# Performance work log

Measured on AMD Instinct MI355X. Metric: run time of the kernel, lower is better.

The kernel has to match this reference:

```python
import jax, jax.numpy as jnp
import numpy as np

K = 4  # neighbors per node (loop=False, PyG knn_graph default)

def _leaky(x):
    return jax.nn.leaky_relu(x, negative_slope=0.01)

def _knn(pos):
    # pos: [B, N, 3]. k nearest neighbors per node within its own graph, no self-loops.
    d = jnp.sum((pos[:, :, None, :] - pos[:, None, :, :]) ** 2, axis=-1)  # [B, N, N]
    n = pos.shape[1]
    d = jnp.where(jnp.eye(n, dtype=bool), jnp.inf, d)
    _, idx = jax.lax.top_k(-d, K)
    return idx  # [B, N, K] neighbor (source) indices per center node

def _edge_conv(x, idx, w1, b1, w2, b2):
    # PyG EdgeConv, aggr='add': out_i = sum_j MLP(concat[x_i, x_j - x_i])
    xj = jax.vmap(lambda xb, ib: xb[ib])(x, idx)  # gather neighbors -> [B, N, K, F]
    xi = x[:, :, None, :]
    e = jnp.concatenate([jnp.broadcast_to(xi, xj.shape), xj - xi], axis=-1)  # [B,N,K,2F]
    h = _leaky(_leaky(e @ w1 + b1) @ w2 + b2)
    return h.sum(axis=2)  # scatter-add over the K neighbors -> [B, N, F_out]

# l1=4, l2=96, l3=192, l4=252, l5=192, l6=96, l7=1  (input_size=4, c=3, output_size=1)
PARAM_SHAPES = [
    ("c1w1", (8, 96)), ("c1b1", (96,)), ("c1w2", (96, 192)), ("c1b2", (192,)),
    ("c2w1", (384, 252)), ("c2b1", (252,)), ("c2w2", (252, 192)), ("c2b2", (192,)),
    ("c3w1", (384, 252)), ("c3b1", (252,)), ("c3w2", (252, 192)), ("c3b2", (192,)),
    ("c4w1", (384, 252)), ("c4b1", (252,)), ("c4w2", (252, 192)), ("c4b2", (192,)),
    ("nn1w", (772, 252)), ("nn1b", (252,)),
    ("nn2w", (252, 192)), ("nn2b", (192,)),
    ("nn3w", (768, 96)), ("nn3b", (96,)),
    ("nn4w", (96, 1)), ("nn4b", (1,)),
]

def setup_inputs():
    key = jax.random.key(0)
    B, N, F = 256, 256, 4  # 256 graphs x 256 nodes, 4 node features
    inp = {"x": jax.random.normal(key, (B, N, F), jnp.float32)}
    for i, (name, shp) in enumerate(PARAM_SHAPES):
        k = jax.random.fold_in(key, i + 1)
        scale = 1.0 / np.sqrt(shp[0]) if len(shp) == 2 else 0.01
        inp[name] = jax.random.normal(k, shp, jnp.float32) * scale
    return inp

def reference(x, c1w1, c1b1, c1w2, c1b2, c2w1, c2b1, c2w2, c2b2,
              c3w1, c3b1, c3w2, c3b2, c4w1, c4b1, c4w2, c4b2,
              nn1w, nn1b, nn2w, nn2b, nn3w, nn3b, nn4w, nn4b):
    # 4 rounds of (dynamic kNN on first 3 feature cols) + EdgeConv(add)
    a = _edge_conv(x, _knn(x[..., :3]), c1w1, c1b1, c1w2, c1b2)
    b = _edge_conv(a, _knn(a[..., :3]), c2w1, c2b1, c2w2, c2b2)
    c = _edge_conv(b, _knn(b[..., :3]), c3w1, c3b1, c3w2, c3b2)
    d = _edge_conv(c, _knn(c[..., :3]), c4w1, c4b1, c4w2, c4b2)
    h = jnp.concatenate([x, a, b, c, d], axis=-1)  # [B, N, 4 + 4*192 = 772]
    h = _leaky(h @ nn1w + nn1b)
    h = h @ nn2w + nn2b  # [B, N, 192]
    # four-way global pooling per graph: max / min / sum / mean
    pooled = jnp.concatenate(
        [h.max(axis=1), h.min(axis=1), h.sum(axis=1), h.mean(axis=1)], axis=-1)  # [B, 768]
    out = _leaky(pooled)
    out = _leaky(out @ nn3w + nn3b)
    return out @ nn4w + nn4b  # [B, 1] (mode='custom': no tanh)
```

## Files before the change

### kernel.cpp

```cpp
#include <hip/hip_runtime.h>
#include <cstdint>
#include <cstddef>

#define LK(x) ((x) > 0.f ? (x) : 0.01f * (x))

typedef _Float16 f16x8 __attribute__((ext_vector_type(8)));
typedef _Float16 f16x4 __attribute__((ext_vector_type(4)));
typedef float f32x4 __attribute__((ext_vector_type(4)));

constexpr int B_ = 256;
constexpr int N_ = 256;
constexpr int BN = B_ * N_;
constexpr int CHUNK_B = 64;
constexpr int CHUNK_ROWS = CHUNK_B * N_;

__device__ inline void dec2(float v, _Float16& h, _Float16& l) {
  _Float16 hh = (_Float16)v;
  h = hh;
  l = (_Float16)(v - (float)hh);
}

__global__ void knn_kernel(const float* __restrict__ feat, int F, int* __restrict__ idxout) {
  __shared__ float px[N_], py[N_], pz[N_];
  int b = blockIdx.x, t = threadIdx.x;
  const float* row = feat + ((size_t)b * N_ + t) * F;
  px[t] = row[0]; py[t] = row[1]; pz[t] = row[2];
  __syncthreads();
  float x = px[t], y = py[t], z = pz[t];
  float bd0 = INFINITY, bd1 = INFINITY, bd2 = INFINITY, bd3 = INFINITY;
  int bi0 = 0, bi1 = 0, bi2 = 0, bi3 = 0;
  for (int j = 0; j < N_; ++j) {
    #pragma clang fp contract(off)
    float dx = x - px[j], dy = y - py[j], dz = z - pz[j];
    float d = (dx * dx + dy * dy) + dz * dz;
    if (j == t) continue;
    if (d < bd3) {
      if (d < bd2) {
        bd3 = bd2; bi3 = bi2;
        if (d < bd1) {
          bd2 = bd1; bi2 = bi1;
          if (d < bd0) { bd1 = bd0; bi1 = bi0; bd0 = d; bi0 = j; }
          else         { bd1 = d; bi1 = j; }
        } else         { bd2 = d; bi2 = j; }
      } else           { bd3 = d; bi3 = j; }
    }
  }
  int* o = idxout + ((size_t)b * N_ + t) * 4;
  o[0] = bi0; o[1] = bi1; o[2] = bi2; o[3] = bi3;
}


__global__ void prep_uvw(const float* __restrict__ w1, const float* __restrict__ b1,
                         int F, int H1, float* __restrict__ wcat, float* __restrict__ bcat) {
  int t = blockIdx.x * 256 + threadIdx.x;
  int FH = F * H1;
  if (t < FH) {
    int k = t / H1, c = t - k * H1;
    float top = w1[(size_t)k * H1 + c];
    float bot = w1[(size_t)(F + k) * H1 + c];
    wcat[(size_t)k * 2 * H1 + c]      = top - bot;
    wcat[(size_t)k * 2 * H1 + H1 + c] = bot;
  }
  if (t < H1) { bcat[t] = b1[t]; bcat[H1 + t] = 0.f; }
}

template<bool ACT_A, bool ACCUM, bool HAS_BIAS>
__global__ __launch_bounds__(256) void gemm_f32(
    const float* __restrict__ A, const float* __restrict__ W,
    const float* __restrict__ bias, float* __restrict__ C,
    int M, int N, int K) {
  __shared__ float sA[16][132];
  __shared__ float sW[16][68];
  int tid = threadIdx.x;
  int m0 = blockIdx.y * 128;
  int n0 = blockIdx.x * 64;
  int kkA = tid & 15, mA = tid >> 4;
  int nW = tid & 63, kW = tid >> 6;
  int ty = tid >> 4, tx = tid & 15;
  float acc[8][4] = {};
  for (int k0 = 0; k0 < K; k0 += 16) {
    int kg = k0 + kkA;
    #pragma unroll
    for (int i = 0; i < 8; ++i) {
      int m = mA + i * 16;
      float v = 0.f;
      if (kg < K) {
        v = A[(size_t)(m0 + m) * K + kg];
        if (ACT_A) v = LK(v);
      }
      sA[kkA][m] = v;
    }
    #pragma unroll
    for (int q = 0; q < 4; ++q) {
      int kk = kW + q * 4;
      int kgw = k0 + kk, n = n0 + nW;
      float v = 0.f;
      if (kgw < K && n < N) v = W[(size_t)kgw * N + n];
      sW[kk][nW] = v;
    }
    __syncthreads();
    #pragma unroll
    for (int kk = 0; kk < 16; ++kk) {
      float4 a0 = *(const float4*)&sA[kk][ty * 8];
      float4 a1 = *(const float4*)&sA[kk][ty * 8 + 4];
      float4 w  = *(const float4*)&sW[kk][tx * 4];
      float av[8] = {a0.x, a0.y, a0.z, a0.w, a1.x, a1.y, a1.z, a1.w};
      float wv[4] = {w.x, w.y, w.z, w.w};
      #pragma unroll
      for (int i = 0; i < 8; ++i)
        #pragma unroll
        for (int j = 0; j < 4; ++j)
          acc[i][j] += av[i] * wv[j];
    }
    __syncthreads();
  }
  int n = n0 + tx * 4;
  float bv[4] = {0.f, 0.f, 0.f, 0.f};
  if (HAS_BIAS) {
    #pragma unroll
    for (int j = 0; j < 4; ++j) if (n + j < N) bv[j] = bias[n + j];
  }
  #pragma unroll
  for (int i = 0; i < 8; ++i) {
    size_t m = (size_t)(m0 + ty * 8 + i);
    if (n + 3 < N) {
      float4 o;
      o.x = acc[i][0] + bv[0]; o.y = acc[i][1] + bv[1];
      o.z = acc[i][2] + bv[2]; o.w = acc[i][3] + bv[3];
      float4* cp = (float4*)(C + m * N + n);
      if (ACCUM) { float4 c = *cp; o.x += c.x; o.y += c.y; o.z += c.z; o.w += c.w; }
      *cp = o;
    } else {
      #pragma unroll
      for (int j = 0; j < 4; ++j) {
        if (n + j < N) {
          float v = acc[i][j] + bv[j];
          size_t off = m * N + n + j;
          if (ACCUM) v += C[off];
          C[off] = v;
        }
      }
    }
  }
}

__global__ __launch_bounds__(256) void edge_stage2(
    const float* __restrict__ UV, const int* __restrict__ idx,
    const float* __restrict__ w2, const float* __restrict__ b2,
    float* __restrict__ out, int H1) {
  __shared__ float sH[16][68];
  __shared__ float sW[16][196];
  __shared__ int sJ[64];
  int tid = threadIdx.x;
  int g0 = blockIdx.x * 16;
  int bbase = (g0 >> 8) << 8;
  if (tid < 64) sJ[tid] = bbase + idx[(size_t)g0 * 4 + tid];
  int W2 = H1 * 2;
  int r = tid >> 2, seg = tid & 3;
  int gp_r = g0 + (r >> 2);
  int ty = tid >> 4, tx = tid & 15;
  int gp = g0 + ty;
  float acc[4][12] = {};
  int nKt = (H1 + 15) >> 4;
  for (int kt = 0; kt < nKt; ++kt) {
    int k0 = kt << 4;
    __syncthreads();
    {
      int c = k0 + (seg << 2);
      const float* up = UV + (size_t)gp_r * W2 + c;
      const float* vp = UV + (size_t)sJ[r] * W2 + H1 + c;
      float u[4], v[4];
      if (c + 3 < H1) {
        float4 uu = *(const float4*)up; float4 vv = *(const float4*)vp;
        u[0] = uu.x; u[1] = uu.y; u[2] = uu.z; u[3] = uu.w;
        v[0] = vv.x; v[1] = vv.y; v[2] = vv.z; v[3] = vv.w;
      } else {
        #pragma unroll
        for (int j = 0; j < 4; ++j) {
          u[j] = (c + j < H1) ? up[j] : 0.f;
          v[j] = (c + j < H1) ? vp[j] : 0.f;
        }
      }
      #pragma unroll
      for (int j = 0; j < 4; ++j) {
        float t = u[j] + v[j];
        sH[(seg << 2) + j][r] = (c + j < H1) ? LK(t) : 0.f;
      }
    }
    #pragma unroll
    for (int p = 0; p < 3; ++p) {
      int q = tid + (p << 8);
      int kk = q / 48;
      int c4 = q - kk * 48;
      int k = k0 + kk;
      float4 wv = {0.f, 0.f, 0.f, 0.f};
      if (k < H1) wv = *(const float4*)(w2 + (size_t)k * 192 + (c4 << 2));
      *(float4*)&sW[kk][c4 << 2] = wv;
    }
    __syncthreads();
    #pragma unroll
    for (int kk = 0; kk < 16; ++kk) {
      float4 a = *(const float4*)&sH[kk][ty << 2];
      float av[4] = {a.x, a.y, a.z, a.w};
      #pragma unroll
      for (int ct = 0; ct < 3; ++ct) {
        float4 w = *(const float4*)&sW[kk][ct * 64 + (tx << 2)];
        float wv[4] = {w.x, w.y, w.z, w.w};
        #pragma unroll
        for (int i = 0; i < 4; ++i)
          #pragma unroll
          for (int j = 0; j < 4; ++j)
            acc[i][ct * 4 + j] += av[i] * wv[j];
      }
    }
  }
  #pragma unroll
  for (int ct = 0; ct < 3; ++ct) {
    float o[4];
    #pragma unroll
    for (int j = 0; j < 4; ++j) {
      int col = ct * 64 + (tx << 2) + j;
      float bvv = b2[col];
      float s = 0.f;
      #pragma unroll
      for (int i = 0; i < 4; ++i) {
        float t = acc[i][ct * 4 + j] + bvv;
        s += LK(t);
      }
      o[j] = s;
    }
    float4 ov = {o[0], o[1], o[2], o[3]};
    *(float4*)(out + (size_t)gp * 192 + ct * 64 + (tx << 2)) = ov;
  }
}


__global__ void prep_wcatT(const float* __restrict__ w1, const float* __restrict__ b1,
                           int F, int H1, int Fpad, _Float16* __restrict__ Wp,
                           float* __restrict__ bcat) {
  int t = blockIdx.x * 256 + threadIdx.x;
  int NN = 2 * H1;
  if (t < NN * Fpad) {
    int n = t / Fpad, k = t - n * Fpad;
    float v = 0.f;
    if (k < F) {
      if (n < H1) v = w1[(size_t)k * H1 + n] - w1[(size_t)(F + k) * H1 + n];
      else        v = w1[(size_t)(F + k) * H1 + (n - H1)];
    }
    _Float16 h, l; dec2(v, h, l);
    size_t base = (size_t)n * 2 * Fpad + (size_t)(k >> 3) * 16 + (k & 7);
    Wp[base] = h; Wp[base + 8] = l;
  }
  if (t < NN) bcat[t] = (t < H1) ? b1[t] : 0.f;
}

__global__ void prep_wT(const float* __restrict__ W, int K, int N, int Kpad,
                        _Float16* __restrict__ Wp) {
  int t = blockIdx.x * 256 + threadIdx.x;
  if (t >= N * Kpad) return;
  int n = t / Kpad, k = t - n * Kpad;
  float v = (k < K) ? W[(size_t)k * N + n] : 0.f;
  _Float16 h, l; dec2(v, h, l);
  size_t base = (size_t)n * 2 * Kpad + (size_t)(k >> 3) * 16 + (k & 7);
  Wp[base] = h; Wp[base + 8] = l;
}

template<bool ACT_A, bool ACCUM, bool HAS_BIAS>
__global__ __launch_bounds__(256) void gemm3h(
    const float* __restrict__ A0, const float* __restrict__ A1, int w0,
    const _Float16* __restrict__ Wp, const float* __restrict__ bias,
    float* __restrict__ C, int M, int N, int K, int Kpad) {
  __shared__ _Float16 sA[128 * 72];
  __shared__ _Float16 sB[128 * 72];
  int tid = threadIdx.x;
  int m0 = blockIdx.y * 128, n0 = blockIdx.x * 128;
  int lane = tid & 63, wid = tid >> 6;
  int wy = wid >> 1, wx = wid & 1;
  int lm = lane & 15, lq = lane >> 4;
  int rA = tid >> 1, qA = (tid & 1) * 4;
  f32x4 acc[4][4];
  #pragma unroll
  for (int i = 0; i < 4; ++i)
    #pragma unroll
    for (int j = 0; j < 4; ++j) acc[i][j] = 0.f;

  for (int k0 = 0; k0 < Kpad; k0 += 32) {
    __syncthreads();
    {
      const float* Ap; int kb, wA;
      if (k0 < w0) { Ap = A0; kb = k0;      wA = w0; }
      else         { Ap = A1; kb = k0 - w0; wA = K - w0; }
      const float* arow = Ap + (size_t)(m0 + rA) * wA;
      #pragma unroll
      for (int qi = 0; qi < 4; ++qi) {
        int q = qA + qi;
        int kl = kb + q * 4;
        float4 v = {0.f, 0.f, 0.f, 0.f};
        if (kl + 3 < wA) v = *(const float4*)(arow + kl);
        else {
          if (kl + 0 < wA) v.x = arow[kl + 0];
          if (kl + 1 < wA) v.y = arow[kl + 1];
          if (kl + 2 < wA) v.z = arow[kl + 2];
        }
        if (ACT_A) { v.x = LK(v.x); v.y = LK(v.y); v.z = LK(v.z); v.w = LK(v.w); }
        _Float16 h0,h1,h2,h3,l0,l1,l2,l3;
        dec2(v.x,h0,l0); dec2(v.y,h1,l1); dec2(v.z,h2,l2); dec2(v.w,h3,l3);
        int off = rA * 72 + (q >> 1) * 16 + (q & 1) * 4;
        f16x4 th; th[0]=h0; th[1]=h1; th[2]=h2; th[3]=h3;
        f16x4 tl; tl[0]=l0; tl[1]=l1; tl[2]=l2; tl[3]=l3;
        *(f16x4*)&sA[off]     = th;
        *(f16x4*)&sA[off + 8] = tl;
      }
    }
    {
      int n = n0 + rA;
      const _Float16* src = Wp + (size_t)n * 2 * Kpad + (size_t)k0 * 2;
      #pragma unroll
      for (int ui = 0; ui < 4; ++ui) {
        int u = (tid & 1) * 4 + ui;
        float4 v = {0.f, 0.f, 0.f, 0.f};
        if (n < N) v = *(const float4*)(src + u * 8);
        *(float4*)&sB[rA * 72 + u * 8] = v;
      }
    }
    __syncthreads();
    f16x8 af[4][2], bf[4][2];
    #pragma unroll
    for (int mt = 0; mt < 4; ++mt) {
      int row = wy * 64 + mt * 16 + lm;
      af[mt][0] = *(const f16x8*)&sA[row * 72 + lq * 16];
      af[mt][1] = *(const f16x8*)&sA[row * 72 + lq * 16 + 8];
    }
    #pragma unroll
    for (int nt = 0; nt < 4; ++nt) {
      int row = wx * 64 + nt * 16 + lm;
      bf[nt][0] = *(const f16x8*)&sB[row * 72 + lq * 16];
      bf[nt][1] = *(const f16x8*)&sB[row * 72 + lq * 16 + 8];
    }
    #pragma unroll
    for (int mt = 0; mt < 4; ++mt)
      #pragma unroll
      for (int nt = 0; nt < 4; ++nt) {
        acc[mt][nt] = __builtin_amdgcn_mfma_f32_16x16x32_f16(af[mt][0], bf[nt][0], acc[mt][nt], 0, 0, 0);
        acc[mt][nt] = __builtin_amdgcn_mfma_f32_16x16x32_f16(af[mt][0], bf[nt][1], acc[mt][nt], 0, 0, 0);
        acc[mt][nt] = __builtin_amdgcn_mfma_f32_16x16x32_f16(af[mt][1], bf[nt][0], acc[mt][nt], 0, 0, 0);
      }
  }
  #pragma unroll
  for (int mt = 0; mt < 4; ++mt) {
    #pragma unroll
    for (int nt = 0; nt < 4; ++nt) {
      int n = n0 + wx * 64 + nt * 16 + lm;
      if (n >= N) continue;
      float bv = HAS_BIAS ? bias[n] : 0.f;
      #pragma unroll
      for (int r = 0; r < 4; ++r) {
        size_t m = (size_t)m0 + wy * 64 + mt * 16 + lq * 4 + r;
        float v = acc[mt][nt][r] + bv;
        size_t off = m * N + n;
        if (ACCUM) v += C[off];
        C[off] = v;
      }
    }
  }
}

__global__ __launch_bounds__(256) void edge_stage2_m(
    const float* __restrict__ UV, const int* __restrict__ idx,
    const _Float16* __restrict__ Wp, const float* __restrict__ b2,
    float* __restrict__ out, int H1, int Kpad) {
  __shared__ _Float16 sH[64 * 72];
  __shared__ _Float16 sW[192 * 72];
  __shared__ int sJ[64];
  int tid = threadIdx.x;
  int g0 = blockIdx.x * 16;
  int bbase = (g0 >> 8) << 8;
  if (tid < 64) sJ[tid] = bbase + idx[(size_t)g0 * 4 + tid];
  int W2 = 2 * H1;
  int lane = tid & 63, w = tid >> 6;
  int lm = lane & 15, lq = lane >> 4;
  int rS = tid >> 2, qS = tid & 3;
  f32x4 acc[4][3];
  #pragma unroll
  for (int i = 0; i < 4; ++i)
    #pragma unroll
    for (int j = 0; j < 3; ++j) acc[i][j] = 0.f;

  for (int k0 = 0; k0 < Kpad; k0 += 32) {
    __syncthreads();
    {
      int gp_r = g0 + (rS >> 2);
      int jr = sJ[rS];
      const float* up = UV + (size_t)gp_r * W2;
      const float* vp = UV + (size_t)jr * W2 + H1;
      #pragma unroll
      for (int hf = 0; hf < 2; ++hf) {
        int k = k0 + qS * 8 + hf * 4;
        float4 u = {0.f,0.f,0.f,0.f}, v = {0.f,0.f,0.f,0.f};
        if (k + 3 < H1) { u = *(const float4*)(up + k); v = *(const float4*)(vp + k); }
        else {
          if (k + 0 < H1) { u.x = up[k+0]; v.x = vp[k+0]; }
          if (k + 1 < H1) { u.y = up[k+1]; v.y = vp[k+1]; }
          if (k + 2 < H1) { u.z = up[k+2]; v.z = vp[k+2]; }
        }
        float e0 = LK(u.x + v.x), e1 = LK(u.y + v.y), e2 = LK(u.z + v.z), e3 = LK(u.w + v.w);
        _Float16 h0,h1,h2,h3,l0,l1,l2,l3;
        dec2(e0,h0,l0); dec2(e1,h1,l1); dec2(e2,h2,l2); dec2(e3,h3,l3);
        int off = rS * 72 + qS * 16 + hf * 4;
        f16x4 th; th[0]=h0; th[1]=h1; th[2]=h2; th[3]=h3;
        f16x4 tl; tl[0]=l0; tl[1]=l1; tl[2]=l2; tl[3]=l3;
        *(f16x4*)&sH[off]     = th;
        *(f16x4*)&sH[off + 8] = tl;
      }
    }
    {
      const _Float16* src = Wp + (size_t)k0 * 2;
      #pragma unroll
      for (int p = 0; p < 6; ++p) {
        int e = tid + p * 256;
        int n = e >> 3, u = e & 7;
        *(float4*)&sW[n * 72 + u * 8] =
            *(const float4*)(src + (size_t)n * 2 * Kpad + u * 8);
      }
    }
    __syncthreads();
    f16x8 af[4][2], bf[3][2];
    #pragma unroll
    for (int mt = 0; mt < 4; ++mt) {
      int row = mt * 16 + lm;
      af[mt][0] = *(const f16x8*)&sH[row * 72 + lq * 16];
      af[mt][1] = *(const f16x8*)&sH[row * 72 + lq * 16 + 8];
    }
    #pragma unroll
    for (int t3 = 0; t3 < 3; ++t3) {
      int row = (w * 3 + t3) * 16 + lm;
      bf[t3][0] = *(const f16x8*)&sW[row * 72 + lq * 16];
      bf[t3][1] = *(const f16x8*)&sW[row * 72 + lq * 16 + 8];
    }
    #pragma unroll
    for (int mt = 0; mt < 4; ++mt)
      #pragma unroll
      for (int t3 = 0; t3 < 3; ++t3) {
        acc[mt][t3] = __builtin_amdgcn_mfma_f32_16x16x32_f16(af[mt][0], bf[t3][0], acc[mt][t3], 0, 0, 0);
        acc[mt][t3] = __builtin_amdgcn_mfma_f32_16x16x32_f16(af[mt][0], bf[t3][1], acc[mt][t3], 0, 0, 0);
        acc[mt][t3] = __builtin_amdgcn_mfma_f32_16x16x32_f16(af[mt][1], bf[t3][0], acc[mt][t3], 0, 0, 0);
      }
  }
  #pragma unroll
  for (int mt = 0; mt < 4; ++mt) {
    int gp = g0 + mt * 4 + lq;
    #pragma unroll
    for (int t3 = 0; t3 < 3; ++t3) {
      int col = (w * 3 + t3) * 16 + lm;
      float bv = b2[col];
      float s = 0.f;
      #pragma unroll
      for (int r = 0; r < 4; ++r) s += LK(acc[mt][t3][r] + bv);
      out[(size_t)gp * 192 + col] = s;
    }
  }
}

__global__ __launch_bounds__(256) void nn1_init(const float* __restrict__ x,
                                                const float* __restrict__ Wx,
                                                const float* __restrict__ b,
                                                float* __restrict__ h1) {
  __shared__ float sX[64][4];
  __shared__ float sW[4][256];
  int tid = threadIdx.x;
  int r0 = blockIdx.x * 64;
  if (tid < 64) *(float4*)sX[tid] = *(const float4*)(x + (size_t)(r0 + tid) * 4);
  for (int e = tid; e < 1024; e += 256) {
    int k = e >> 8, n = e & 255;
    sW[k][n] = (n < 252) ? Wx[(size_t)k * 252 + n] : 0.f;
  }
  __syncthreads();
  int cg = tid & 63, rr = tid >> 6;
  if (cg < 63) {
    #pragma unroll 4
    for (int i = 0; i < 16; ++i) {
      int rl = rr + i * 4;
      float x0 = sX[rl][0], x1 = sX[rl][1], x2 = sX[rl][2], x3 = sX[rl][3];
      float4 o;
      int c = cg * 4;
      o.x = b[c+0] + x0*sW[0][c+0] + x1*sW[1][c+0] + x2*sW[2][c+0] + x3*sW[3][c+0];
      o.y = b[c+1] + x0*sW[0][c+1] + x1*sW[1][c+1] + x2*sW[2][c+1] + x3*sW[3][c+1];
      o.z = b[c+2] + x0*sW[0][c+2] + x1*sW[1][c+2] + x2*sW[2][c+2] + x3*sW[3][c+2];
      o.w = b[c+3] + x0*sW[0][c+3] + x1*sW[1][c+3] + x2*sW[2][c+3] + x3*sW[3][c+3];
      *(float4*)(h1 + (size_t)(r0 + rl) * 252 + c) = o;
    }
  }
}

__global__ void pool_kernel(const float* __restrict__ h, float* __restrict__ pooled) {
  int b = blockIdx.x, ch = threadIdx.x;
  const float* p = h + (size_t)b * N_ * 192 + ch;
  float mx = -INFINITY, mn = INFINITY, sm = 0.f;
  for (int n = 0; n < N_; ++n) {
    float v = p[(size_t)n * 192];
    mx = fmaxf(mx, v); mn = fminf(mn, v); sm += v;
  }
  float* o = pooled + (size_t)b * 768;
  o[ch]       = LK(mx);
  o[192 + ch] = LK(mn);
  o[384 + ch] = LK(sm);
  o[576 + ch] = LK(sm * (1.f / 256.f));
}

__global__ void head_kernel(const float* __restrict__ pooled,
                            const float* __restrict__ w3, const float* __restrict__ b3,
                            const float* __restrict__ w4, const float* __restrict__ b4,
                            float* __restrict__ out) {
  __shared__ float sp[768];
  __shared__ float st[96];
  int b = blockIdx.x, t = threadIdx.x;
  for (int c = t; c < 768; c += 128) sp[c] = pooled[(size_t)b * 768 + c];
  __syncthreads();
  if (t < 96) {
    float s = b3[t];
    for (int r = 0; r < 768; ++r) s += sp[r] * w3[(size_t)r * 96 + t];
    s = LK(s);
    st[t] = s * w4[t];
  }
  __syncthreads();
  if (t == 0) {
    float s = b4[0];
    for (int i = 0; i < 96; ++i) s += st[i];
    out[b] = s;
  }
}

extern "C" void kernel_launch(void* const* d_in, const int* in_sizes, int n_in,
                              void* d_out, int out_size, void* d_ws, size_t ws_size,
                              hipStream_t stream) {
  (void)in_sizes; (void)n_in; (void)out_size; (void)ws_size;
  const float* x = (const float*)d_in[0];
  const float* P[25];
  for (int i = 0; i < 25; ++i) P[i] = (const float*)d_in[i];

  char* ws = (char*)d_ws;
  int*       idx    = (int*)      (ws + 0);
  float*     A      = (float*)    (ws + 1048576);
  float*     Bb     = (float*)    (ws + 51380224);
  float*     h1     = (float*)    (ws + 101711872);
  float*     UV     = (float*)    (ws + 167772160);
  float*     pooled = (float*)    (ws + 200802304);
  char*      WSH1   =             (ws + 201588736);
  _Float16*  WB2    = (_Float16*) (ws + 202113024);
  float*     bcat   = (float*)    (ws + 202637312);

  float*    wcat = (float*)   WSH1;
  _Float16* WB1  = (_Float16*)WSH1;

  auto edge_layer_f32 = [&](const float* src, int F, int H1,
                            const float* w1, const float* b1,
                            const float* w2, const float* b2, float* dst) {
    knn_kernel<<<B_, N_, 0, stream>>>(src, F, idx);
    prep_uvw<<<(F * H1 + 255) / 256, 256, 0, stream>>>(w1, b1, F, H1, wcat, bcat);
    int W2 = 2 * H1;
    dim3 gUV((W2 + 63) / 64, CHUNK_ROWS / 128);
    for (int cb = 0; cb < B_; cb += CHUNK_B) {
      size_t base = (size_t)cb * N_;
      gemm_f32<false, false, true><<<gUV, 256, 0, stream>>>(src + base * F, wcat, bcat, UV, CHUNK_ROWS, W2, F);
      edge_stage2<<<CHUNK_ROWS / 16, 256, 0, stream>>>(UV, idx + base * 4, w2, b2, dst + base * 192, H1);
    }
  };

  auto edge_layer_f16 = [&](const float* src, int F, int H1,
                            const float* w1, const float* b1,
                            const float* w2, const float* b2, float* dst) {
    int Fpad = (F + 31) & ~31;
    int KpadW2 = (H1 + 31) & ~31;
    int NN = 2 * H1;
    knn_kernel<<<B_, N_, 0, stream>>>(src, F, idx);
    prep_wcatT<<<(NN * Fpad + 255) / 256, 256, 0, stream>>>(w1, b1, F, H1, Fpad, WB1, bcat);
    prep_wT<<<(192 * KpadW2 + 255) / 256, 256, 0, stream>>>(w2, H1, 192, KpadW2, WB2);
    dim3 gUV((NN + 127) / 128, CHUNK_ROWS / 128);
    for (int cb = 0; cb < B_; cb += CHUNK_B) {
      size_t base = (size_t)cb * N_;
      gemm3h<false, false, true><<<gUV, 256, 0, stream>>>(
          src + base * F, src + base * F, F, WB1, bcat, UV, CHUNK_ROWS, NN, F, Fpad);
      edge_stage2_m<<<CHUNK_ROWS / 16, 256, 0, stream>>>(
          UV, idx + base * 4, WB2, b2, dst + base * 192, H1, KpadW2);
    }
  };

  edge_layer_f32(x,  4,   96,  P[1], P[2], P[3], P[4], A);
  edge_layer_f32(A,  192, 252, P[5], P[6], P[7], P[8], Bb);

  nn1_init<<<BN / 64, 256, 0, stream>>>(x, P[17], P[18], h1);
  {
    prep_wT<<<(252 * 384 + 255) / 256, 256, 0, stream>>>(P[17] + 4 * 252, 384, 252, 384, WB1);
    dim3 g(2, BN / 128);
    gemm3h<false, true, false><<<g, 256, 0, stream>>>(A, Bb, 192, WB1, nullptr, h1, BN, 252, 384, 384);
  }

  edge_layer_f32(Bb, 192, 252, P[9],  P[10], P[11], P[12], A);
  edge_layer_f16(A,  192, 252, P[13], P[14], P[15], P[16], Bb);

  {
    prep_wT<<<(252 * 384 + 255) / 256, 256, 0, stream>>>(P[17] + (size_t)388 * 252, 384, 252, 384, WB1);
    dim3 g(2, BN / 128);
    gemm3h<false, true, false><<<g, 256, 0, stream>>>(A, Bb, 192, WB1, nullptr, h1, BN, 252, 384, 384);
  }

  {
    prep_wT<<<(192 * 256 + 255) / 256, 256, 0, stream>>>(P[19], 252, 192, 256, WB2);
    dim3 g(2, BN / 128);
    gemm3h<true, false, true><<<g, 256, 0, stream>>>(h1, h1, 252, WB2, P[20], A, BN, 192, 252, 256);
  }

  pool_kernel<<<B_, 192, 0, stream>>>(A, pooled);
  head_kernel<<<B_, 128, 0, stream>>>(pooled, P[21], P[22], P[23], P[24], (float*)d_out);
}
```

Baseline: 2.199 ms.

## Use f16 MFMA stage2 for layer 3 with exact fp32 recompute of knn columns

Layer 3's second edge-conv stage now runs on the split-f16 MFMA kernel instead of the fp32 stage2. A new edge_exact3 kernel then recomputes the first three output columns in fp32 and overwrites them, because those columns drive the next layer's kNN and must stay exact. Separately, the nn1_init kernel is folded into the first h1 GEMM epilogue, which adds the x-times-Wx term and the bias directly. The change adds an extra pass over UV for the three columns and depends on the f16 split being accurate enough for the remaining columns.

```diff
diff --git a/kernel.cpp b/kernel.cpp
--- a/kernel.cpp
+++ b/kernel.cpp
@@ -234,6 +234,63 @@
   }
 }
 
+__global__ __launch_bounds__(256) void edge_exact3(
+    const float* __restrict__ UV, const int* __restrict__ idx,
+    const float* __restrict__ w2, const float* __restrict__ b2,
+    float* __restrict__ out, int H1) {
+  __shared__ float sw[252 * 4];
+  int tid = threadIdx.x;
+  for (int k = tid; k < H1; k += 256) {
+    sw[k * 4 + 0] = w2[(size_t)k * 192 + 0];
+    sw[k * 4 + 1] = w2[(size_t)k * 192 + 1];
+    sw[k * 4 + 2] = w2[(size_t)k * 192 + 2];
+    sw[k * 4 + 3] = 0.f;
+  }
+  __syncthreads();
+  int p = blockIdx.x * 64 + (tid >> 2);
+  int e = tid & 3;
+  int bbase = (p >> 8) << 8;
+  int j = bbase + idx[(size_t)p * 4 + e];
+  int W2 = 2 * H1;
+  const float* up = UV + (size_t)p * W2;
+  const float* vp = UV + (size_t)j * W2 + H1;
+  float a0 = 0.f, a1 = 0.f, a2 = 0.f;
+  int k = 0;
+  for (; k + 3 < H1; k += 4) {
+    float4 u = *(const float4*)(up + k);
+    float4 v = *(const float4*)(vp + k);
+    float h0 = LK(u.x + v.x), h1 = LK(u.y + v.y);
+    float h2 = LK(u.z + v.z), h3 = LK(u.w + v.w);
+    float4 w0 = *(const float4*)&sw[(k + 0) * 4];
+    float4 w1 = *(const float4*)&sw[(k + 1) * 4];
+    float4 w2v = *(const float4*)&sw[(k + 2) * 4];
+    float4 w3 = *(const float4*)&sw[(k + 3) * 4];
+    a0 = __builtin_fmaf(h0, w0.x, a0); a1 = __builtin_fmaf(h0, w0.y, a1); a2 = __builtin_fmaf(h0, w0.z, a2);
+    a0 = __builtin_fmaf(h1, w1.x, a0); a1 = __builtin_fmaf(h1, w1.y, a1); a2 = __builtin_fmaf(h1, w1.z, a2);
+    a0 = __builtin_fmaf(h2, w2v.x, a0); a1 = __builtin_fmaf(h2, w2v.y, a1); a2 = __builtin_fmaf(h2, w2v.z, a2);
+    a0 = __builtin_fmaf(h3, w3.x, a0); a1 = __builtin_fmaf(h3, w3.y, a1); a2 = __builtin_fmaf(h3, w3.z, a2);
+  }
+  for (; k < H1; ++k) {
+    float h = LK(up[k] + vp[k]);
+    a0 = __builtin_fmaf(h, sw[k * 4 + 0], a0);
+    a1 = __builtin_fmaf(h, sw[k * 4 + 1], a1);
+    a2 = __builtin_fmaf(h, sw[k * 4 + 2], a2);
+  }
+  float acc3[3] = {a0, a1, a2};
+  #pragma unroll
+  for (int c = 0; c < 3; ++c) {
+    float t = acc3[c] + b2[c];
+    float pc = LK(t);
+    float q1 = __shfl_down(pc, 1);
+    float q2 = __shfl_down(pc, 2);
+    float q3 = __shfl_down(pc, 3);
+    if (e == 0) {
+      float s = ((pc + q1) + q2) + q3;
+      out[(size_t)p * 192 + c] = s;
+    }
+  }
+}
+
 
 __global__ void prep_wcatT(const float* __restrict__ w1, const float* __restrict__ b1,
                            int F, int H1, int Fpad, _Float16* __restrict__ Wp,
@@ -265,10 +322,11 @@
   Wp[base] = h; Wp[base + 8] = l;
 }
 
-template<bool ACT_A, bool ACCUM, bool HAS_BIAS>
+template<bool ACT_A, bool ACCUM, bool HAS_BIAS, bool XB>
 __global__ __launch_bounds__(256) void gemm3h(
     const float* __restrict__ A0, const float* __restrict__ A1, int w0,
     const _Float16* __restrict__ Wp, const float* __restrict__ bias,
+    const float* __restrict__ X, const float* __restrict__ Wx,
     float* __restrict__ C, int M, int N, int K, int Kpad) {
   __shared__ _Float16 sA[128 * 72];
   __shared__ _Float16 sB[128 * 72];
@@ -346,6 +404,25 @@
         acc[mt][nt] = __builtin_amdgcn_mfma_f32_16x16x32_f16(af[mt][1], bf[nt][0], acc[mt][nt], 0, 0, 0);
       }
   }
+  if (XB) {
+    #pragma unroll
+    for (int mt = 0; mt < 4; ++mt) {
+      #pragma unroll
+      for (int r = 0; r < 4; ++r) {
+        size_t m = (size_t)m0 + wy * 64 + mt * 16 + lq * 4 + r;
+        float4 xv = *(const float4*)(X + m * 4);
+        #pragma unroll
+        for (int nt = 0; nt < 4; ++nt) {
+          int n = n0 + wx * 64 + nt * 16 + lm;
+          if (n >= N) continue;
+          float v = acc[mt][nt][r] + bias[n]
+                  + (xv.x * Wx[n] + xv.y * Wx[N + n] + xv.z * Wx[2 * N + n] + xv.w * Wx[3 * N + n]);
+          C[m * N + n] = v;
+        }
+      }
+    }
+    return;
+  }
   #pragma unroll
   for (int mt = 0; mt < 4; ++mt) {
     #pragma unroll
@@ -461,37 +538,6 @@
   }
 }
 
-__global__ __launch_bounds__(256) void nn1_init(const float* __restrict__ x,
-                                                const float* __restrict__ Wx,
-                                                const float* __restrict__ b,
-                                                float* __restrict__ h1) {
-  __shared__ float sX[64][4];
-  __shared__ float sW[4][256];
-  int tid = threadIdx.x;
-  int r0 = blockIdx.x * 64;
-  if (tid < 64) *(float4*)sX[tid] = *(const float4*)(x + (size_t)(r0 + tid) * 4);
-  for (int e = tid; e < 1024; e += 256) {
-    int k = e >> 8, n = e & 255;
-    sW[k][n] = (n < 252) ? Wx[(size_t)k * 252 + n] : 0.f;
-  }
-  __syncthreads();
-  int cg = tid & 63, rr = tid >> 6;
-  if (cg < 63) {
-    #pragma unroll 4
-    for (int i = 0; i < 16; ++i) {
-      int rl = rr + i * 4;
-      float x0 = sX[rl][0], x1 = sX[rl][1], x2 = sX[rl][2], x3 = sX[rl][3];
-      float4 o;
-      int c = cg * 4;
-      o.x = b[c+0] + x0*sW[0][c+0] + x1*sW[1][c+0] + x2*sW[2][c+0] + x3*sW[3][c+0];
-      o.y = b[c+1] + x0*sW[0][c+1] + x1*sW[1][c+1] + x2*sW[2][c+1] + x3*sW[3][c+1];
-      o.z = b[c+2] + x0*sW[0][c+2] + x1*sW[1][c+2] + x2*sW[2][c+2] + x3*sW[3][c+2];
-      o.w = b[c+3] + x0*sW[0][c+3] + x1*sW[1][c+3] + x2*sW[2][c+3] + x3*sW[3][c+3];
-      *(float4*)(h1 + (size_t)(r0 + rl) * 252 + c) = o;
-    }
-  }
-}
-
 __global__ void pool_kernel(const float* __restrict__ h, float* __restrict__ pooled) {
   int b = blockIdx.x, ch = threadIdx.x;
   const float* p = h + (size_t)b * N_ * 192 + ch;
@@ -539,18 +585,19 @@
   for (int i = 0; i < 25; ++i) P[i] = (const float*)d_in[i];
 
   char* ws = (char*)d_ws;
-  int*       idx    = (int*)      (ws + 0);
-  float*     A      = (float*)    (ws + 1048576);
-  float*     Bb     = (float*)    (ws + 51380224);
-  float*     h1     = (float*)    (ws + 101711872);
-  float*     UV     = (float*)    (ws + 167772160);
-  float*     pooled = (float*)    (ws + 200802304);
-  char*      WSH1   =             (ws + 201588736);
-  _Float16*  WB2    = (_Float16*) (ws + 202113024);
-  float*     bcat   = (float*)    (ws + 202637312);
-
-  float*    wcat = (float*)   WSH1;
-  _Float16* WB1  = (_Float16*)WSH1;
+  int*   idx    = (int*)  (ws + 0);
+  float* A      = (float*)(ws + 1048576);
+  float* Bb     = (float*)(ws + 51380224);
+  float* h1     = (float*)(ws + 101711872);
+  float* UV     = (float*)(ws + 167772160);
+  float* pooled = (float*)(ws + 200802304);
+  char*  Wsl1   =         (ws + 201588736);
+  char*  Wsl2   =         (ws + 202637312);
+  float* bcat   = (float*)(ws + 203685888);
+
+  float*    wcat = (float*)   Wsl1;
+  _Float16* WB1  = (_Float16*)Wsl1;
+  _Float16* WB2  = (_Float16*)Wsl2;
 
   auto edge_layer_f32 = [&](const float* src, int F, int H1,
                             const float* w1, const float* b1,
@@ -578,8 +625,8 @@
     dim3 gUV((NN + 127) / 128, CHUNK_ROWS / 128);
     for (int cb = 0; cb < B_; cb += CHUNK_B) {
       size_t base = (size_t)cb * N_;
-      gemm3h<false, false, true><<<gUV, 256, 0, stream>>>(
-          src + base * F, src + base * F, F, WB1, bcat, UV, CHUNK_ROWS, NN, F, Fpad);
+      gemm3h<false, false, true, false><<<gUV, 256, 0, stream>>>(
+          src + base * F, src + base * F, F, WB1, bcat, nullptr, nullptr, UV, CHUNK_ROWS, NN, F, Fpad);
       edge_stage2_m<<<CHUNK_ROWS / 16, 256, 0, stream>>>(
           UV, idx + base * 4, WB2, b2, dst + base * 192, H1, KpadW2);
     }
@@ -588,26 +635,45 @@
   edge_layer_f32(x,  4,   96,  P[1], P[2], P[3], P[4], A);
   edge_layer_f32(A,  192, 252, P[5], P[6], P[7], P[8], Bb);
 
-  nn1_init<<<BN / 64, 256, 0, stream>>>(x, P[17], P[18], h1);
   {
     prep_wT<<<(252 * 384 + 255) / 256, 256, 0, stream>>>(P[17] + 4 * 252, 384, 252, 384, WB1);
     dim3 g(2, BN / 128);
-    gemm3h<false, true, false><<<g, 256, 0, stream>>>(A, Bb, 192, WB1, nullptr, h1, BN, 252, 384, 384);
-  }
-
-  edge_layer_f32(Bb, 192, 252, P[9],  P[10], P[11], P[12], A);
-  edge_layer_f16(A,  192, 252, P[13], P[14], P[15], P[16], Bb);
+    gemm3h<false, false, true, true><<<g, 256, 0, stream>>>(
+        A, Bb, 192, WB1, P[18], x, P[17], h1, BN, 252, 384, 384);
+  }
+
+  {
+    const float* src = Bb;
+    const float* w1 = P[9]; const float* b1 = P[10];
+    const float* w2 = P[11]; const float* b2 = P[12];
+    float* dst = A;
+    int F = 192, H1 = 252, W2 = 504, KpadW2 = 256;
+    knn_kernel<<<B_, N_, 0, stream>>>(src, F, idx);
+    prep_uvw<<<(F * H1 + 255) / 256, 256, 0, stream>>>(w1, b1, F, H1, wcat, bcat);
+    prep_wT<<<(192 * KpadW2 + 255) / 256, 256, 0, stream>>>(w2, H1, 192, KpadW2, WB2);
+    dim3 gUV((W2 + 63) / 64, CHUNK_ROWS / 128);
+    for (int cb = 0; cb < B_; cb += CHUNK_B) {
+      size_t base = (size_t)cb * N_;
+      gemm_f32<false, false, true><<<gUV, 256, 0, stream>>>(src + base * F, wcat, bcat, UV, CHUNK_ROWS, W2, F);
+      edge_stage2_m<<<CHUNK_ROWS / 16, 256, 0, stream>>>(UV, idx + base * 4, WB2, b2, dst + base * 192, H1, KpadW2);
+      edge_exact3<<<CHUNK_ROWS / 64, 256, 0, stream>>>(UV, idx + base * 4, w2, b2, dst + base * 192, H1);
+    }
+  }
+
+  edge_layer_f16(A, 192, 252, P[13], P[14], P[15], P[16], Bb);
 
   {
     prep_wT<<<(252 * 384 + 255) / 256, 256, 0, stream>>>(P[17] + (size_t)388 * 252, 384, 252, 384, WB1);
     dim3 g(2, BN / 128);
-    gemm3h<false, true, false><<<g, 256, 0, stream>>>(A, Bb, 192, WB1, nullptr, h1, BN, 252, 384, 384);
+    gemm3h<false, true, false, false><<<g, 256, 0, stream>>>(
+        A, Bb, 192, WB1, nullptr, nullptr, nullptr, h1, BN, 252, 384, 384);
   }
 
   {
     prep_wT<<<(192 * 256 + 255) / 256, 256, 0, stream>>>(P[19], 252, 192, 256, WB2);
     dim3 g(2, BN / 128);
-    gemm3h<true, false, true><<<g, 256, 0, stream>>>(h1, h1, 252, WB2, P[20], A, BN, 192, 252, 256);
+    gemm3h<true, false, true, false><<<g, 256, 0, stream>>>(
+        h1, h1, 252, WB2, P[20], nullptr, nullptr, A, BN, 192, 252, 256);
   }
 
   pool_kernel<<<B_, 192, 0, stream>>>(A, pooled);
```

Result: faster. 2.062 ms (median of 2 runs) (-6.2%).
